# Performance work log

Measured on AMD Instinct MI355X. Metric: run time of the kernel, lower is better.

The kernel has to match this reference:

```python
import jax, jax.numpy as jnp
from jax import lax
import numpy as np

N = 20000   # nodes
D = 16      # padded max in-degree
E = 2       # edge types
F = 128     # in_feats = hidden_size (DGL LSTM hidden size == in feats)
C = 2       # num_classes


def setup_inputs() -> dict:
    key = jax.random.key(0)
    ks = jax.random.split(key, 20)
    s = 0.08  # small init scale for stability
    p = lambda k, shape: jax.random.normal(k, shape, jnp.float32) * s
    return {
        "x": jax.random.normal(ks[0], (N, F), jnp.float32),
        "nbr": jax.random.randint(ks[1], (E, N, D), 0, N),
        "deg": jax.random.randint(ks[2], (E, N), 0, D + 1),
        "l1_Wih": p(ks[3], (E, F, 4 * F)),
        "l1_Whh": p(ks[4], (E, F, 4 * F)),
        "l1_bih": p(ks[5], (E, 4 * F)),
        "l1_bhh": p(ks[6], (E, 4 * F)),
        "l1_Wself": p(ks[7], (E, F, F)),
        "l1_Wneigh": p(ks[8], (E, F, F)),
        "l1_b": p(ks[9], (E, F)),
        "l2_Wih": p(ks[10], (E, F, 4 * F)),
        "l2_Whh": p(ks[11], (E, F, 4 * F)),
        "l2_bih": p(ks[12], (E, 4 * F)),
        "l2_bhh": p(ks[13], (E, 4 * F)),
        "l2_Wself": p(ks[14], (E, F, C)),
        "l2_Wneigh": p(ks[15], (E, F, C)),
        "l2_b": p(ks[16], (E, C)),
    }


def _lstm_agg(seq, mask, Wih, Whh, bih, bhh):
    """Masked LSTM reduction over padded neighbor sequences.
    seq: [N, D, F] gathered neighbor feats; mask: [N, D] bool (step < deg).
    Returns final hidden state [N, F] (zeros for zero-degree nodes)."""
    n, _, f = seq.shape
    h0 = jnp.zeros((n, f), seq.dtype)

    def step(carry, inputs):
        h, c = carry
        x_t, m_t = inputs  # [N,F], [N,1]
        gates = x_t @ Wih + bih + h @ Whh + bhh  # [N,4F]
        i, fg, g, o = jnp.split(gates, 4, axis=-1)  # torch gate order i,f,g,o
        c_new = jax.nn.sigmoid(fg) * c + jax.nn.sigmoid(i) * jnp.tanh(g)
        h_new = jax.nn.sigmoid(o) * jnp.tanh(c_new)
        return (jnp.where(m_t, h_new, h), jnp.where(m_t, c_new, c)), None

    xs = (jnp.swapaxes(seq, 0, 1), jnp.swapaxes(mask, 0, 1)[..., None])
    (h_fin, _), _ = lax.scan(step, (h0, h0), xs)
    return h_fin


def _hetero_sage_layer(h, nbr, deg, Wih, Whh, bih, bhh, Wself, Wneigh, b):
    """HeteroGraphConv(mean) over E SAGEConv(lstm) layers, single node type."""
    n_et = nbr.shape[0]
    d = nbr.shape[2]
    steps = jnp.arange(d)[None, :]
    out = 0.0
    for e in range(n_et):  # small fixed loop over edge types
        seq = h[nbr[e]]                     # [N, D, F] irregular gather
        mask = steps < deg[e][:, None]      # [N, D]
        h_neigh = _lstm_agg(seq, mask, Wih[e], Whh[e], bih[e], bhh[e])
        out = out + (h @ Wself[e] + h_neigh @ Wneigh[e] + b[e])
    return out / n_et


def reference(x, nbr, deg,
              l1_Wih, l1_Whh, l1_bih, l1_bhh, l1_Wself, l1_Wneigh, l1_b,
              l2_Wih, l2_Whh, l2_bih, l2_bhh, l2_Wself, l2_Wneigh, l2_b):
    h = jax.nn.relu(_hetero_sage_layer(x, nbr, deg, l1_Wih, l1_Whh, l1_bih,
                                       l1_bhh, l1_Wself, l1_Wneigh, l1_b))
    logits = _hetero_sage_layer(h, nbr, deg, l2_Wih, l2_Whh, l2_bih, l2_bhh,
                                l2_Wself, l2_Wneigh, l2_b)
    return (logits, jax.nn.softmax(logits, axis=1))
```

## Files before the change

### kernel.cpp

```cpp
#include <hip/hip_runtime.h>
#include <stdint.h>

#define NN 20000
#define DD 16
#define FF 128
#define GG 512

typedef _Float16 h16;
typedef _Float16 half8 __attribute__((ext_vector_type(8)));
typedef float f32x4 __attribute__((ext_vector_type(4)));
typedef float f32x16 __attribute__((ext_vector_type(16)));

#define OFF_X    0u
#define OFF_H1   5120000u
#define OFF_N1   10240000u
#define OFF_N2   20480000u
#define OFF_B1   30720000u
#define OFF_WC1  31768576u
#define OFF_WC2  31866880u
#define OFF_BI1  31869952u
#define OFF_BI2  31874048u
#define OFF_BS1  31878144u
#define OFF_B2S  31878656u
#define OFF_PERM 31878912u
#define OFF_HIST 32039168u
#define OFF_CUR  32039424u

__device__ __forceinline__ float sigm(float x)  { return __builtin_amdgcn_rcpf(1.f + __expf(-x)); }
__device__ __forceinline__ float tanh_(float x) { return 2.f * __builtin_amdgcn_rcpf(1.f + __expf(-2.f * x)) - 1.f; }

__device__ __forceinline__ void gload_lds16(const void* g, void* s) {
    __builtin_amdgcn_global_load_lds((const __attribute__((address_space(1))) void*)g,
                                     (__attribute__((address_space(3))) void*)s, 16, 0, 0);
}

__device__ __forceinline__ half8 load_afrag16(const unsigned short* Asrc, int rowbase,
                                              int ll, int lg, int kcL) {
    int row = rowbase + ll;
    int o = (kcL * 64 + lg * 16) ^ ((row & 7) << 4);
    return *(const half8*)((const char*)Asrc + row * 256 + o);
}

__global__ void k_prep(const float* __restrict__ x, h16* __restrict__ xo,
                       const float* __restrict__ l1Wih, const float* __restrict__ l1Whh,
                       const float* __restrict__ l2Wih, const float* __restrict__ l2Whh,
                       h16* __restrict__ Bp,
                       const float* __restrict__ l1Ws, const float* __restrict__ l1Wn,
                       h16* __restrict__ Cp,
                       const float* __restrict__ l1bih, const float* __restrict__ l1bhh,
                       const float* __restrict__ l2bih, const float* __restrict__ l2bhh,
                       const float* __restrict__ l1b,  const float* __restrict__ l2Ws,
                       const float* __restrict__ l2Wn, const float* __restrict__ l2b,
                       float* __restrict__ bias1, float* __restrict__ bias2,
                       float* __restrict__ bs1,  float* __restrict__ wc2,
                       float* __restrict__ b2s,
                       const int* __restrict__ deg, int* __restrict__ hist) {
    const int b = blockIdx.x, tid = threadIdx.x;
    if (b < 1250) {
        int base = (b * 256 + tid) * 8;
        const float4* p = (const float4*)(x + base);
        float4 a = p[0], c = p[1];
        half8 v = {(h16)a.x,(h16)a.y,(h16)a.z,(h16)a.w,(h16)c.x,(h16)c.y,(h16)c.z,(h16)c.w};
        *(half8*)(xo + base) = v;
    } else if (b < 1506) {
        int idx = (b - 1250) * 256 + tid;
        int set = idx >> 14;
        int rem = idx & 16383;
        int w   = rem >> 10;
        int kc  = (rem >> 6) & 15;
        int l   = rem & 63;
        const float* Wih = (set < 2 ? l1Wih : l2Wih) + (size_t)(set & 1) * (FF * GG);
        const float* Whh = (set < 2 ? l1Whh : l2Whh) + (size_t)(set & 1) * (FF * GG);
        int rl   = l & 31;
        int gate = rl >> 3, fl = rl & 7;
        int col  = gate * 128 + w * 8 + fl;
        int hi   = l >> 5;
        half8 v;
#pragma unroll
        for (int j = 0; j < 8; j++) {
            int k = kc * 16 + 8 * hi + j;
            float val = (k < FF) ? Wih[k * GG + col] : Whh[(k - FF) * GG + col];
            v[j] = (h16)val;
        }
        *(half8*)(Bp + (size_t)idx * 8) = v;
    } else if (b < 1530) {
        int idx = (b - 1506) * 256 + tid;
        int kc = idx >> 9;
        int ct = (idx >> 6) & 7;
        int l  = idx & 63;
        int col = ct * 16 + (l & 15);
        half8 v;
#pragma unroll
        for (int j = 0; j < 8; j++) {
            int k = kc * 32 + ((l >> 4) << 3) + j;
            float val;
            if (k < 128)      val = 0.5f * (l1Ws[k * 128 + col] + l1Ws[16384 + k * 128 + col]);
            else if (k < 256) val = 0.5f * l1Wn[(k - 128) * 128 + col];
            else              val = 0.5f * l1Wn[16384 + (k - 256) * 128 + col];
            v[j] = (h16)val;
        }
        *(half8*)(Cp + (size_t)idx * 8) = v;
    } else if (b < 1538) {
        int g = (b - 1530) * 256 + tid;
        if (g < 1024) bias1[g] = l1bih[g] + l1bhh[g];
        else if (g < 2048) { int j = g - 1024; bias2[j] = l2bih[j] + l2bhh[j]; }
        if (g < 128) bs1[g] = 0.5f * (l1b[g] + l1b[128 + g]);
        if (g < 768) {
            int k = g >> 1, c = g & 1;
            float val;
            if (k < 128)      val = 0.5f * (l2Ws[k * 2 + c] + l2Ws[256 + k * 2 + c]);
            else if (k < 256) val = 0.5f * l2Wn[(k - 128) * 2 + c];
            else              val = 0.5f * l2Wn[16384 >= 512 ? (k - 256) * 2 + c : 0];
            if (k >= 256)     val = 0.5f * l2Wn[256 + (k - 256) * 2 + c];
            wc2[g] = val;
        }
        if (g < 2) b2s[g] = 0.5f * (l2b[g] + l2b[2 + g]);
    } else {
        int bb = b - 1538;
        int e = bb / 79;
        int n = (bb % 79) * 256 + tid;
        if (n < NN) atomicAdd(&hist[e * 32 + deg[(size_t)e * NN + n]], 1);
    }
}

__global__ void k_scan(const int* __restrict__ hist, int* __restrict__ cursor) {
    int e = threadIdx.x;
    if (e < 2) {
        int acc = 0;
        for (int d = 16; d >= 0; d--) { cursor[e * 32 + d] = acc; acc += hist[e * 32 + d]; }
    }
}
__global__ void k_scatter(const int* __restrict__ deg, int* __restrict__ cursor,
                          int* __restrict__ perm) {
    int e = blockIdx.y; int n = blockIdx.x * 256 + threadIdx.x;
    if (n < NN) {
        int d = deg[(size_t)e * NN + n];
        int p = atomicAdd(&cursor[e * 32 + d], 1);
        perm[(size_t)e * NN + p] = n;
    }
}

__global__ __launch_bounds__(1024, 4)
void k_lstm(const h16* __restrict__ src, const int* __restrict__ nbr_g,
            const int* __restrict__ deg_g, const h16* __restrict__ Bp_g,
            const float* __restrict__ bias_g, const int* __restrict__ perm_g,
            h16* __restrict__ out_g) {
    const int bx = blockIdx.x;
    const int e = bx & 1;
    const int node0 = (bx >> 1) * 32;
    const int* nbr  = nbr_g  + (size_t)e * NN * DD;
    const int* deg  = deg_g  + (size_t)e * NN;
    const int* perm = perm_g + (size_t)e * NN;
    const h16* Bp   = Bp_g + (size_t)e * 131072u;
    const float* bias = bias_g + e * GG;
    h16* outp = out_g + (size_t)e * NN * FF;

    __shared__ unsigned short Axb[2][32 * 128];
    __shared__ unsigned short Ahb[2][32 * 128];
    __shared__ int nbr_l[32 * DD];

    const int tid = threadIdx.x;
    const int l = tid & 63, w = tid >> 6;
    const int hi = l >> 5, col = l & 31;

    if (tid < 512) {
        int node = node0 + (tid >> 4);
        nbr_l[tid] = nbr[(size_t)perm[node] * DD + (tid & 15)];
    }
    *(uint2*)&Ahb[0][tid * 4] = make_uint2(0, 0);

    const int pn    = perm[node0 + col];
    const int degl  = deg[pn];
    const int tmax  = deg[perm[node0]];

    f32x16 biasv;
#pragma unroll
    for (int r = 0; r < 16; r++)
        biasv[r] = bias[(r >> 2) * 128 + w * 8 + (r & 3) + 4 * hi];

    if (degl == 0)
        *(uint2*)&outp[(size_t)pn * FF + w * 8 + 4 * hi] = make_uint2(0, 0);

    half8 breg[16];
#pragma unroll
    for (int kc = 0; kc < 16; kc++)
        breg[kc] = *(const half8*)(Bp + ((size_t)(w * 16 + kc) * 64 + l) * 8);

    float cst[4] = {0.f, 0.f, 0.f, 0.f};

    const int swz   = (col & 15) << 4;
    const int vbase = col * 256 + ((hi * 16) ^ swz);
    const int hwoff = col * 256 + (((w * 16 + 8 * hi)) ^ swz);

    auto do_gather = [&](int t1, unsigned short* dst) {
        if (w < 8) {
            int row = w * 4 + (l >> 4);
            int idx = nbr_l[row * DD + t1];
            const char* gp = (const char*)(src + (size_t)idx * FF)
                             + (((l & 15) * 16) ^ ((row & 15) << 4));
            gload_lds16(gp, &dst[(w * 4) * 128]);
        }
    };

    __syncthreads();
    do_gather(0, Axb[0]);
    __syncthreads();

#pragma unroll 1
    for (int t = 0; t < tmax; t++) {
        const int cur = t & 1, nxt = cur ^ 1;
        if (t + 1 < tmax) do_gather(t + 1, Axb[nxt]);

        f32x16 acc;
        {
            half8 bf = *(const half8*)((const char*)Axb[cur] + vbase);
            acc = __builtin_amdgcn_mfma_f32_32x32x16_f16(breg[0], bf, biasv, 0, 0, 0);
        }
#pragma unroll
        for (int kc = 1; kc < 16; kc++) {
            const char* S = (kc < 8) ? (const char*)Axb[cur] : (const char*)Ahb[cur];
            half8 bf = *(const half8*)(S + (vbase ^ ((kc & 7) * 32)));
            acc = __builtin_amdgcn_mfma_f32_32x32x16_f16(breg[kc], bf, acc, 0, 0, 0);
        }

        unsigned int hlo, hhi2;
        {
            unsigned short hq[4];
#pragma unroll
            for (int q = 0; q < 4; q++) {
                float iv = sigm(acc[q]);
                float fv = sigm(acc[4 + q]);
                float gv = tanh_(acc[8 + q]);
                float ov = sigm(acc[12 + q]);
                float c_ = fv * cst[q] + iv * gv;
                float h_ = ov * tanh_(c_);
                cst[q] = c_;
                h16 hh = (h16)h_;
                hq[q] = __builtin_bit_cast(unsigned short, hh);
            }
            hlo  = (unsigned int)hq[0] | ((unsigned int)hq[1] << 16);
            hhi2 = (unsigned int)hq[2] | ((unsigned int)hq[3] << 16);
        }
        *(uint2*)((char*)Ahb[nxt] + hwoff) = make_uint2(hlo, hhi2);
        if (t + 1 == degl)
            *(uint2*)&outp[(size_t)pn * FF + w * 8 + 4 * hi] = make_uint2(hlo, hhi2);

        __syncthreads();
    }
}

__global__ __launch_bounds__(256, 4)
void k_lout1(const h16* __restrict__ x16, const h16* __restrict__ n0,
             const h16* __restrict__ n1, const h16* __restrict__ Cp,
             const float* __restrict__ bs, h16* __restrict__ h1) {
    __shared__ unsigned short A3[3][64 * 128];
    const int tid = threadIdx.x;
    const int l = tid & 63, w = tid >> 6, lg = l >> 4, ll = l & 15;
    const int node0 = blockIdx.x * 64;
    const h16* srcs[3] = {x16, n0, n1};
#pragma unroll
    for (int r3 = 0; r3 < 3; r3++)
#pragma unroll
        for (int k = 0; k < 4; k++) {
            int row = w * 16 + k * 4 + lg;
            int node = node0 + row;
            uint4 v = (node < NN) ? *(const uint4*)(srcs[r3] + (size_t)node * FF + ll * 8)
                                  : make_uint4(0, 0, 0, 0);
            *(uint4*)((char*)&A3[r3][0] + row * 256 + ((ll * 16) ^ ((row & 7) << 4))) = v;
        }
    __syncthreads();

    f32x4 acc[4][2];
#pragma unroll
    for (int rt = 0; rt < 4; rt++)
#pragma unroll
        for (int ct = 0; ct < 2; ct++) {
            float b = bs[(w * 2 + ct) * 16 + ll];
            acc[rt][ct] = (f32x4){b, b, b, b};
        }
#pragma unroll
    for (int kc = 0; kc < 12; kc++) {
        const unsigned short* Asrc = &A3[kc >> 2][0];
        int kcL = kc & 3;
        half8 af[4];
#pragma unroll
        for (int rt = 0; rt < 4; rt++) af[rt] = load_afrag16(Asrc, rt * 16, ll, lg, kcL);
        half8 bf[2];
#pragma unroll
        for (int ct = 0; ct < 2; ct++)
            bf[ct] = *(const half8*)(Cp + ((size_t)(kc * 8 + w * 2 + ct) * 64 + l) * 8);
#pragma unroll
        for (int rt = 0; rt < 4; rt++)
#pragma unroll
            for (int ct = 0; ct < 2; ct++)
                acc[rt][ct] = __builtin_amdgcn_mfma_f32_16x16x32_f16(af[rt], bf[ct], acc[rt][ct], 0, 0, 0);
    }
#pragma unroll
    for (int rt = 0; rt < 4; rt++)
#pragma unroll
        for (int ct = 0; ct < 2; ct++)
#pragma unroll
            for (int r = 0; r < 4; r++) {
                int node = node0 + rt * 16 + (lg << 2) + r;
                if (node < NN) {
                    float v = acc[rt][ct][r];
                    v = v > 0.f ? v : 0.f;
                    h1[(size_t)node * FF + (w * 2 + ct) * 16 + ll] = (h16)v;
                }
            }
}

__global__ void k_lout2(const h16* __restrict__ h1, const h16* __restrict__ n0,
                        const h16* __restrict__ n1, const float* __restrict__ wc2,
                        const float* __restrict__ b2s, float* __restrict__ out) {
    __shared__ float Wl[768];
    const int tid = threadIdx.x;
    for (int i = tid; i < 768; i += 256) Wl[i] = wc2[i];
    __syncthreads();
    const int node = blockIdx.x * 64 + (tid >> 2);
    const int q = tid & 3;
    float a0 = 0.f, a1 = 0.f;
    if (node < NN) {
        const h16* srcs[3] = {h1, n0, n1};
#pragma unroll
        for (int r3 = 0; r3 < 3; r3++) {
            const h16* sp = srcs[r3] + (size_t)node * FF + q * 32;
#pragma unroll
            for (int c4 = 0; c4 < 4; c4++) {
                half8 v = *(const half8*)(sp + c4 * 8);
#pragma unroll
                for (int i = 0; i < 8; i++) {
                    float xv = (float)v[i];
                    int k = r3 * 128 + q * 32 + c4 * 8 + i;
                    a0 += xv * Wl[k * 2];
                    a1 += xv * Wl[k * 2 + 1];
                }
            }
        }
    }
    a0 += __shfl_xor(a0, 1); a0 += __shfl_xor(a0, 2);
    a1 += __shfl_xor(a1, 1); a1 += __shfl_xor(a1, 2);
    if (q == 0 && node < NN) {
        a0 += b2s[0]; a1 += b2s[1];
        out[(size_t)node * 2]     = a0;
        out[(size_t)node * 2 + 1] = a1;
        float m = fmaxf(a0, a1);
        float e0 = __expf(a0 - m), e1 = __expf(a1 - m);
        float s = 1.f / (e0 + e1);
        out[40000 + (size_t)node * 2]     = e0 * s;
        out[40000 + (size_t)node * 2 + 1] = e1 * s;
    }
}

extern "C" void kernel_launch(void* const* d_in, const int* in_sizes, int n_in,
                              void* d_out, int out_size, void* d_ws, size_t ws_size,
                              hipStream_t stream) {
    const float* x     = (const float*)d_in[0];
    const int*   nbr   = (const int*)d_in[1];
    const int*   deg   = (const int*)d_in[2];
    const float* l1Wih = (const float*)d_in[3];
    const float* l1Whh = (const float*)d_in[4];
    const float* l1bih = (const float*)d_in[5];
    const float* l1bhh = (const float*)d_in[6];
    const float* l1Ws  = (const float*)d_in[7];
    const float* l1Wn  = (const float*)d_in[8];
    const float* l1b   = (const float*)d_in[9];
    const float* l2Wih = (const float*)d_in[10];
    const float* l2Whh = (const float*)d_in[11];
    const float* l2bih = (const float*)d_in[12];
    const float* l2bhh = (const float*)d_in[13];
    const float* l2Ws  = (const float*)d_in[14];
    const float* l2Wn  = (const float*)d_in[15];
    const float* l2b   = (const float*)d_in[16];

    char* ws = (char*)d_ws;
    h16*  x16   = (h16*)(ws + OFF_X);
    h16*  h1    = (h16*)(ws + OFF_H1);
    h16*  n1b   = (h16*)(ws + OFF_N1);
    h16*  n2b   = (h16*)(ws + OFF_N2);
    h16*  B1    = (h16*)(ws + OFF_B1);
    h16*  B2    = (h16*)(ws + OFF_B1) + 2u * 131072u;
    h16*  Cp1   = (h16*)(ws + OFF_WC1);
    float* wc2  = (float*)(ws + OFF_WC2);
    float* bias1 = (float*)(ws + OFF_BI1);
    float* bias2 = (float*)(ws + OFF_BI2);
    float* bs1   = (float*)(ws + OFF_BS1);
    float* b2s   = (float*)(ws + OFF_B2S);
    int*   perm  = (int*)(ws + OFF_PERM);
    int*   hist  = (int*)(ws + OFF_HIST);
    int*   cur   = (int*)(ws + OFF_CUR);

    hipMemsetAsync(hist, 0, 256, stream);
    k_prep<<<dim3(1696), dim3(256), 0, stream>>>(x, x16,
                                                 l1Wih, l1Whh, l2Wih, l2Whh, B1,
                                                 l1Ws, l1Wn, Cp1,
                                                 l1bih, l1bhh, l2bih, l2bhh,
                                                 l1b, l2Ws, l2Wn, l2b,
                                                 bias1, bias2, bs1, wc2, b2s,
                                                 deg, hist);
    k_scan   <<<dim3(1),     dim3(64),  0, stream>>>(hist, cur);
    k_scatter<<<dim3(79, 2), dim3(256), 0, stream>>>(deg, cur, perm);

    k_lstm <<<dim3(1250), dim3(1024), 0, stream>>>(x16, nbr, deg, B1, bias1, perm, n1b);
    k_lout1<<<dim3(313),  dim3(256),  0, stream>>>(x16, n1b, n1b + (size_t)NN * FF, Cp1, bs1, h1);
    k_lstm <<<dim3(1250), dim3(1024), 0, stream>>>(h1, nbr, deg, B2, bias2, perm, n2b);
    k_lout2<<<dim3(313),  dim3(256),  0, stream>>>(h1, n2b, n2b + (size_t)NN * FF, wc2, b2s,
                                                   (float*)d_out);
}
```

Measured before the change: 494.4 us.

## Replace async global-to-LDS gather with register-prefetched two-deep gather pipeline

The LSTM recurrence kernel stops using global_load_lds DMA for the neighbor feature gather. Each thread now loads its slice into registers two steps ahead and writes it to LDS after the gate math, with a barrier that waits only on lgkmcnt. The final hidden state is kept in registers and stored once at the end instead of conditionally each step, and the bias moves from the MFMA accumulator to a register initializer. This aims to overlap gather latency with the MFMA chain and cut per-step sync cost, at the price of more registers and an unconditional prefetch of padded neighbor indices.

```diff
diff --git a/kernel.cpp b/kernel.cpp
--- a/kernel.cpp
+++ b/kernel.cpp
@@ -29,10 +29,7 @@
 __device__ __forceinline__ float sigm(float x)  { return __builtin_amdgcn_rcpf(1.f + __expf(-x)); }
 __device__ __forceinline__ float tanh_(float x) { return 2.f * __builtin_amdgcn_rcpf(1.f + __expf(-2.f * x)) - 1.f; }
 
-__device__ __forceinline__ void gload_lds16(const void* g, void* s) {
-    __builtin_amdgcn_global_load_lds((const __attribute__((address_space(1))) void*)g,
-                                     (__attribute__((address_space(3))) void*)s, 16, 0, 0);
-}
+#define BAR() asm volatile("s_waitcnt lgkmcnt(0)\n\ts_barrier" ::: "memory")
 
 __device__ __forceinline__ half8 load_afrag16(const unsigned short* Asrc, int rowbase,
                                               int ll, int lg, int kcL) {
@@ -110,8 +107,7 @@
             float val;
             if (k < 128)      val = 0.5f * (l2Ws[k * 2 + c] + l2Ws[256 + k * 2 + c]);
             else if (k < 256) val = 0.5f * l2Wn[(k - 128) * 2 + c];
-            else              val = 0.5f * l2Wn[16384 >= 512 ? (k - 256) * 2 + c : 0];
-            if (k >= 256)     val = 0.5f * l2Wn[256 + (k - 256) * 2 + c];
+            else              val = 0.5f * l2Wn[256 + (k - 256) * 2 + c];
             wc2[g] = val;
         }
         if (g < 2) b2s[g] = 0.5f * (l2b[g] + l2b[2 + g]);
@@ -173,13 +169,10 @@
     const int degl  = deg[pn];
     const int tmax  = deg[perm[node0]];
 
-    f32x16 biasv;
+    float biasr[16];
 #pragma unroll
     for (int r = 0; r < 16; r++)
-        biasv[r] = bias[(r >> 2) * 128 + w * 8 + (r & 3) + 4 * hi];
-
-    if (degl == 0)
-        *(uint2*)&outp[(size_t)pn * FF + w * 8 + 4 * hi] = make_uint2(0, 0);
+        biasr[r] = bias[(r >> 2) * 128 + w * 8 + (r & 3) + 4 * hi];
 
     half8 breg[16];
 #pragma unroll
@@ -187,66 +180,74 @@
         breg[kc] = *(const half8*)(Bp + ((size_t)(w * 16 + kc) * 64 + l) * 8);
 
     float cst[4] = {0.f, 0.f, 0.f, 0.f};
-
-    const int swz   = (col & 15) << 4;
-    const int vbase = col * 256 + ((hi * 16) ^ swz);
-    const int hwoff = col * 256 + (((w * 16 + 8 * hi)) ^ swz);
-
-    auto do_gather = [&](int t1, unsigned short* dst) {
-        if (w < 8) {
-            int row = w * 4 + (l >> 4);
-            int idx = nbr_l[row * DD + t1];
-            const char* gp = (const char*)(src + (size_t)idx * FF)
-                             + (((l & 15) * 16) ^ ((row & 15) << 4));
-            gload_lds16(gp, &dst[(w * 4) * 128]);
-        }
+    uint2 hfin = make_uint2(0, 0);
+
+    const int grow  = 2 * w + hi;
+    const int gcolb = (l & 31) * 8;
+    const int xwoff = grow * 256 + (gcolb ^ ((grow & 15) << 4));
+
+    auto gload = [&](int t1) -> uint2 {
+        int idx = nbr_l[grow * DD + t1];
+        return *(const uint2*)((const char*)src + (size_t)idx * 256 + gcolb);
     };
 
-    __syncthreads();
-    do_gather(0, Axb[0]);
-    __syncthreads();
+    BAR();
+
+    uint2 xr0 = gload(0);
+    uint2 xA  = gload(tmax > 1 ? 1 : 0);
+    *(uint2*)((char*)Axb[0] + xwoff) = xr0;
+    BAR();
+
+    uint2 xB;
+    auto STEP = [&](int t, uint2& xpend, uint2& xfly) {
+        const int cur = t & 1, nxt = cur ^ 1;
+        xfly = gload(t + 2 < DD ? t + 2 : DD - 1);
+
+        f32x16 acc;
+#pragma unroll
+        for (int r = 0; r < 16; r++) acc[r] = biasr[r];
+#pragma unroll
+        for (int kc = 0; kc < 16; kc++) {
+            const char* S = (kc < 8) ? (const char*)Axb[cur] : (const char*)Ahb[cur];
+            int ko = (kc & 7) * 32 + hi * 16;
+            half8 bf = *(const half8*)(S + col * 256 + (ko ^ ((col & 15) << 4)));
+            acc = __builtin_amdgcn_mfma_f32_32x32x16_f16(breg[kc], bf, acc, 0, 0, 0);
+        }
+
+        unsigned short hq[4];
+#pragma unroll
+        for (int q = 0; q < 4; q++) {
+            float iv = sigm(acc[q]);
+            float fv = sigm(acc[4 + q]);
+            float gv = tanh_(acc[8 + q]);
+            float ov = sigm(acc[12 + q]);
+            float c_ = fv * cst[q] + iv * gv;
+            float h_ = ov * tanh_(c_);
+            cst[q] = c_;
+            hq[q] = __builtin_bit_cast(unsigned short, (h16)h_);
+        }
+        uint2 hv;
+        hv.x = (unsigned int)hq[0] | ((unsigned int)hq[1] << 16);
+        hv.y = (unsigned int)hq[2] | ((unsigned int)hq[3] << 16);
+
+        bool fire = (t + 1 == degl);
+        hfin.x = fire ? hv.x : hfin.x;
+        hfin.y = fire ? hv.y : hfin.y;
+
+        int ho = (w * 16 + 8 * hi) ^ ((col & 15) << 4);
+        *(uint2*)((char*)Ahb[nxt] + col * 256 + ho) = hv;
+        *(uint2*)((char*)Axb[nxt] + xwoff) = xpend;
+
+        BAR();
+    };
 
 #pragma unroll 1
-    for (int t = 0; t < tmax; t++) {
-        const int cur = t & 1, nxt = cur ^ 1;
-        if (t + 1 < tmax) do_gather(t + 1, Axb[nxt]);
-
-        f32x16 acc;
-        {
-            half8 bf = *(const half8*)((const char*)Axb[cur] + vbase);
-            acc = __builtin_amdgcn_mfma_f32_32x32x16_f16(breg[0], bf, biasv, 0, 0, 0);
-        }
-#pragma unroll
-        for (int kc = 1; kc < 16; kc++) {
-            const char* S = (kc < 8) ? (const char*)Axb[cur] : (const char*)Ahb[cur];
-            half8 bf = *(const half8*)(S + (vbase ^ ((kc & 7) * 32)));
-            acc = __builtin_amdgcn_mfma_f32_32x32x16_f16(breg[kc], bf, acc, 0, 0, 0);
-        }
-
-        unsigned int hlo, hhi2;
-        {
-            unsigned short hq[4];
-#pragma unroll
-            for (int q = 0; q < 4; q++) {
-                float iv = sigm(acc[q]);
-                float fv = sigm(acc[4 + q]);
-                float gv = tanh_(acc[8 + q]);
-                float ov = sigm(acc[12 + q]);
-                float c_ = fv * cst[q] + iv * gv;
-                float h_ = ov * tanh_(c_);
-                cst[q] = c_;
-                h16 hh = (h16)h_;
-                hq[q] = __builtin_bit_cast(unsigned short, hh);
-            }
-            hlo  = (unsigned int)hq[0] | ((unsigned int)hq[1] << 16);
-            hhi2 = (unsigned int)hq[2] | ((unsigned int)hq[3] << 16);
-        }
-        *(uint2*)((char*)Ahb[nxt] + hwoff) = make_uint2(hlo, hhi2);
-        if (t + 1 == degl)
-            *(uint2*)&outp[(size_t)pn * FF + w * 8 + 4 * hi] = make_uint2(hlo, hhi2);
-
-        __syncthreads();
-    }
+    for (int t = 0; t < tmax; t += 2) {
+        STEP(t, xA, xB);
+        if (t + 1 < tmax) STEP(t + 1, xB, xA);
+    }
+
+    *(uint2*)&outp[(size_t)pn * FF + w * 8 + 4 * hi] = hfin;
 }
 
 __global__ __launch_bounds__(256, 4)
```

After: 915.5 us. 1.85x slower.
